# Kernel optimization log

Hardware: AMD Instinct MI355X
Metric: run time of the kernel (lower is better)

The kernel has to match this reference:

```python
import jax, jax.numpy as jnp
import numpy as np

DT_SCALE = 0.01  # time grid = arange(T) * 0.01, i.e. t in [0, 0.99]


def setup_inputs() -> dict:
    key = jax.random.key(0)
    k1, k2, k3 = jax.random.split(key, 3)
    latents, hidden = 128, 256
    S, N, T = 4, 1024, 100
    first_point = jax.random.normal(k1, (S, N, latents), dtype=jnp.float32)
    time_steps_to_predict = jnp.arange(T, dtype=jnp.float32) * DT_SCALE
    # ODEFunc MLP params (Glorot-ish scaling so tanh stays in a sane range)
    W1 = jax.random.normal(k2, (latents, hidden), dtype=jnp.float32) / np.sqrt(latents)
    b1 = jnp.zeros((hidden,), dtype=jnp.float32)
    W2 = jax.random.normal(k3, (hidden, latents), dtype=jnp.float32) / np.sqrt(hidden)
    b2 = jnp.zeros((latents,), dtype=jnp.float32)
    return {
        "first_point": first_point,
        "time_steps_to_predict": time_steps_to_predict,
        "W1": W1, "b1": b1, "W2": W2, "b2": b2,
    }


def reference(first_point, time_steps_to_predict, W1, b1, W2, b2):
    # ode_func: dy/dt = tanh(y @ W1 + b1) @ W2 + b2 (time-autonomous MLP)
    def f(y):
        return jnp.tanh(y @ W1 + b1) @ W2 + b2

    # torchdiffeq fixed-step 'rk4': one classical RK4 step per output interval.
    t0s = time_steps_to_predict[:-1]
    t1s = time_steps_to_predict[1:]

    def rk4_step(y, ts):
        t0, t1 = ts
        dt = t1 - t0
        half = dt * 0.5
        k1 = f(y)
        k2 = f(y + half * k1)
        k3 = f(y + half * k2)
        k4 = f(y + dt * k3)
        y1 = y + (dt / 6.0) * (k1 + 2.0 * k2 + 2.0 * k3 + k4)
        return y1, y1

    _, ys = jax.lax.scan(rk4_step, first_point, (t0s, t1s))  # [T-1, S, N, D]
    pred_y = jnp.concatenate([first_point[None], ys], axis=0)  # [T, S, N, D]
    # permute(1, 2, 0, 3): [T, S, N, D] -> [S, N, T, D]
    return jnp.transpose(pred_y, (1, 2, 0, 3))
```

## Files before the change

### kernel.cpp

```cpp
#include <hip/hip_runtime.h>
#include <hip/hip_bf16.h>

typedef __attribute__((ext_vector_type(8))) short v8s;
typedef __attribute__((ext_vector_type(4))) float f4;

#define MFMA16(a, b, c) __builtin_amdgcn_mfma_f32_16x16x32_bf16((a), (b), (c), 0, 0, 0)

__device__ __forceinline__ float bf2f(unsigned short u) {
    return __uint_as_float(((unsigned)u) << 16);
}
__device__ __forceinline__ unsigned short f2bf(float x) {
    unsigned u = __float_as_uint(x);
    unsigned r = 0x7FFFu + ((u >> 16) & 1u);
    return (unsigned short)((u + r) >> 16);
}
__device__ __forceinline__ unsigned pack_bf16_2(float a, float b) {
    float2 t; t.x = a; t.y = b;
    union { __hip_bfloat162 h; unsigned u; } cv;
    cv.h = __float22bfloat162_rn(t);
    return cv.u;
}
__device__ __forceinline__ float tanh_scaled(float zs) {
    float u = __builtin_amdgcn_exp2f(zs);
    float r = __builtin_amdgcn_rcpf(u + 1.0f);
    return __builtin_fmaf(-2.0f, r, 1.0f);
}
__device__ __forceinline__ float ldin(const void* p, int i, bool f32) {
    return f32 ? ((const float*)p)[i] : bf2f(((const unsigned short*)p)[i]);
}

#define BROWS 16
#define TSTEPS 100
#define DLAT 128
#define DHID 256
#define HSTR 264
#define HBUF (BROWS * HSTR)
#define TANH_C 2.885390081777927f

__global__ __launch_bounds__(256, 4)
void prep_w21(const void* __restrict__ ts, const void* __restrict__ W1,
              const void* __restrict__ W2, const void* __restrict__ b2,
              void* __restrict__ ws) {
    const bool m32 = fabsf(((const float*)ts)[1] - 0.01f) < 0.004f;
    const int i = blockIdx.x;
    const int j = threadIdx.x;
    float acc = 0.f;
    for (int m = 0; m < DLAT; ++m)
        acc = __builtin_fmaf(ldin(W2, i * DLAT + m, m32), ldin(W1, m * DHID + j, m32), acc);
    ((unsigned short*)ws)[i * DHID + j] = f2bf(TANH_C * acc);
    if (i == 0) {
        float a2 = 0.f;
        for (int m = 0; m < DLAT; ++m)
            a2 = __builtin_fmaf(ldin(b2, m, m32), ldin(W1, m * DHID + j, m32), a2);
        ((float*)((char*)ws + DHID * DHID * 2))[j] = TANH_C * a2;
    }
}

__global__ __launch_bounds__(512, 2)
void ode_rk4_kernel(const void* __restrict__ fp,
                    const void* __restrict__ ts,
                    const void* __restrict__ W1,
                    const void* __restrict__ b1,
                    const void* __restrict__ W2,
                    const void* __restrict__ b2,
                    const void* __restrict__ ws,
                    void* __restrict__ out) {
    __shared__ unsigned short hB[2 * HBUF];
    __shared__ float tsL[TSTEPS];

    const bool m32 = fabsf(((const float*)ts)[1] - 0.01f) < 0.004f;

    const int tid = threadIdx.x;
    const int w = tid >> 6;
    const int lane = tid & 63;
    const int pp = lane & 15;
    const int qq = lane >> 4;
    const int R0 = blockIdx.x * BROWS;

    if (tid < TSTEPS) tsL[tid] = ldin(ts, tid, m32);

    v8s w2f[8];
#pragma unroll
    for (int kt = 0; kt < 8; ++kt) {
        v8s f;
#pragma unroll
        for (int j = 0; j < 8; ++j)
            f[j] = (short)f2bf(ldin(W2, (kt * 32 + qq * 8 + j) * DLAT + 16 * w + pp, m32));
        w2f[kt] = f;
    }
    const unsigned short* w21p = (const unsigned short*)ws;
    v8s w21f[8][2];
#pragma unroll
    for (int kt = 0; kt < 8; ++kt)
#pragma unroll
        for (int nt = 0; nt < 2; ++nt) {
            v8s f;
#pragma unroll
            for (int j = 0; j < 8; ++j)
                f[j] = (short)w21p[(kt * 32 + qq * 8 + j) * DHID + 32 * w + nt * 16 + pp];
            w21f[kt][nt] = f;
        }
    const float* b2w1p = (const float*)((const char*)ws + DHID * DHID * 2);
    const float bz0 = b2w1p[32 * w + pp];
    const float bz1 = b2w1p[32 * w + 16 + pp];
    const float b2v = ldin(b2, 16 * w + pp, m32);

    const int sA = (pp >> 1) & 7;
    int hAoff[8];
#pragma unroll
    for (int kt = 0; kt < 8; ++kt)
        hAoff[kt] = pp * HSTR + (((4 * kt + qq) ^ sA) << 3);
    const int pb = pp >> 3, pw = pp & 7;
    const int s0 = (2 * qq) & 7, s1 = (2 * qq + 1) & 7;
    int hoff[2][2];
    hoff[0][0] = (((4 * w + pb) ^ s0) << 3) + pw;
    hoff[0][1] = (((4 * w + 2 + pb) ^ s0) << 3) + pw;
    hoff[1][0] = (((4 * w + pb) ^ s1) << 3) + pw;
    hoff[1][1] = (((4 * w + 2 + pb) ^ s1) << 3) + pw;

    {
        int row = tid >> 5, ch = tid & 31;
        int sw = (row >> 1) & 7;
        unsigned short* dst = hB + row * HSTR + (((ch >> 1) ^ sw) << 3) + (ch & 1) * 4;
        if (m32) {
            float4 v = *((const float4*)((const float*)fp + (size_t)(R0 + row) * DLAT) + ch);
            *((float4*)((float*)out + ((size_t)(R0 + row) * TSTEPS) * DLAT) + ch) = v;
            ushort4 b; b.x = f2bf(v.x); b.y = f2bf(v.y); b.z = f2bf(v.z); b.w = f2bf(v.w);
            *(ushort4*)dst = b;
        } else {
            const unsigned short* fpu = (const unsigned short*)fp;
            ushort4 v = *((const ushort4*)(fpu + (size_t)(R0 + row) * DLAT) + ch);
            *((ushort4*)((unsigned short*)out + ((size_t)(R0 + row) * TSTEPS) * DLAT) + ch) = v;
            *(ushort4*)dst = v;
        }
    }

    const int c2 = 16 * w + pp;
    float yreg[4];
    size_t ob[4];
#pragma unroll
    for (int r = 0; r < 4; ++r) {
        yreg[r] = ldin(fp, (R0 + 4 * qq + r) * DLAT + c2, m32);
        ob[r] = ((size_t)(R0 + 4 * qq + r) * TSTEPS) * DLAT + c2;
    }

    v8s w1f[4][2];
#pragma unroll
    for (int kt = 0; kt < 4; ++kt)
#pragma unroll
        for (int nt = 0; nt < 2; ++nt) {
            v8s f;
#pragma unroll
            for (int j = 0; j < 8; ++j)
                f[j] = (short)f2bf(TANH_C * ldin(W1, (kt * 32 + qq * 8 + j) * DHID + 32 * w + nt * 16 + pp, m32));
            w1f[kt][nt] = f;
        }
    const float b1s0 = TANH_C * ldin(b1, 32 * w + pp, m32);
    const float b1s1 = TANH_C * ldin(b1, 32 * w + 16 + pp, m32);

    __syncthreads();
    f4 a0 = {0.f, 0.f, 0.f, 0.f}, a1 = {0.f, 0.f, 0.f, 0.f};
#pragma unroll
    for (int kt = 0; kt < 4; ++kt) {
        v8s a = *(const v8s*)(hB + hAoff[kt]);
        a0 = MFMA16(a, w1f[kt][0], a0);
        a1 = MFMA16(a, w1f[kt][1], a1);
    }
    float zs[8];
#pragma unroll
    for (int r = 0; r < 4; ++r) {
        zs[r] = a0[r] + b1s0;
        zs[4 + r] = a1[r] + b1s1;
    }
#pragma unroll
    for (int r = 0; r < 4; ++r) {
        unsigned pu = pack_bf16_2(tanh_scaled(zs[r]), tanh_scaled(zs[4 + r]));
        unsigned short* hp = hB + HBUF + (4 * qq + r) * HSTR;
        hp[hoff[r >> 1][0]] = (unsigned short)pu;
        hp[hoff[r >> 1][1]] = (unsigned short)(pu >> 16);
    }

    for (int t = 0; t < TSTEPS - 1; ++t) {
        const float dt = tsL[t + 1] - tsL[t];
        const float half = 0.5f * dt;
        const float d6 = dt * (1.0f / 6.0f);
        float ksum[4] = {0.f, 0.f, 0.f, 0.f};
        float zsum[8] = {0.f, 0.f, 0.f, 0.f, 0.f, 0.f, 0.f, 0.f};
#pragma unroll
        for (int e = 0; e < 4; ++e) {
            const int rb = (e & 1) ^ 1;
            const int wb = e & 1;
            __syncthreads();
            const unsigned short* hbase = hB + rb * HBUF;
            f4 az0 = {0.f, 0.f, 0.f, 0.f}, az1 = {0.f, 0.f, 0.f, 0.f}, ak = {0.f, 0.f, 0.f, 0.f};
#pragma unroll
            for (int kt = 0; kt < 8; ++kt) {
                v8s a = *(const v8s*)(hbase + hAoff[kt]);
                az0 = MFMA16(a, w21f[kt][0], az0);
                az1 = MFMA16(a, w21f[kt][1], az1);
                ak  = MFMA16(a, w2f[kt], ak);
            }
            const float wgt = (e == 0 || e == 3) ? 1.0f : 2.0f;
            const float cc = (e == 2) ? dt : half;
            float zt[8];
#pragma unroll
            for (int r = 0; r < 4; ++r) {
                float kv = ak[r] + b2v;
                ksum[r] = __builtin_fmaf(wgt, kv, ksum[r]);
                float kz0 = az0[r] + bz0;
                float kz1 = az1[r] + bz1;
                zsum[r]     = __builtin_fmaf(wgt, kz0, zsum[r]);
                zsum[4 + r] = __builtin_fmaf(wgt, kz1, zsum[4 + r]);
                if (e < 3) {
                    zt[r]     = __builtin_fmaf(cc, kz0, zs[r]);
                    zt[4 + r] = __builtin_fmaf(cc, kz1, zs[4 + r]);
                }
            }
            if (e == 3) {
#pragma unroll
                for (int j = 0; j < 8; ++j) {
                    zs[j] = __builtin_fmaf(d6, zsum[j], zs[j]);
                    zt[j] = zs[j];
                }
#pragma unroll
                for (int r = 0; r < 4; ++r)
                    yreg[r] = __builtin_fmaf(d6, ksum[r], yreg[r]);
            }
            unsigned short* wbase = hB + wb * HBUF;
#pragma unroll
            for (int r = 0; r < 4; ++r) {
                unsigned pu = pack_bf16_2(tanh_scaled(zt[r]), tanh_scaled(zt[4 + r]));
                unsigned short* hp = wbase + (4 * qq + r) * HSTR;
                hp[hoff[r >> 1][0]] = (unsigned short)pu;
                hp[hoff[r >> 1][1]] = (unsigned short)(pu >> 16);
            }
        }
        if (m32) {
            float* op = (float*)out;
#pragma unroll
            for (int r = 0; r < 4; ++r)
                op[ob[r] + (size_t)(t + 1) * DLAT] = yreg[r];
        } else {
            unsigned short* op = (unsigned short*)out;
#pragma unroll
            for (int r = 0; r < 4; ++r)
                op[ob[r] + (size_t)(t + 1) * DLAT] = f2bf(yreg[r]);
        }
    }
}

extern "C" void kernel_launch(void* const* d_in, const int* in_sizes, int n_in,
                              void* d_out, int out_size, void* d_ws, size_t ws_size,
                              hipStream_t stream) {
    (void)in_sizes; (void)n_in; (void)out_size; (void)ws_size;
    prep_w21<<<DHID, DHID, 0, stream>>>(d_in[1], d_in[2], d_in[4], d_in[5], d_ws);
    ode_rk4_kernel<<<256, 512, 0, stream>>>(d_in[0], d_in[1], d_in[2], d_in[3],
                                            d_in[4], d_in[5], d_ws, d_out);
}
```

Before: 547.6 us.

## Halve block to four waves, each computing double-width output tiles

The RK4 kernel now launches 256 threads (4 waves) per 16-row block instead of 512. Each wave covers 64 hidden columns and 32 latent columns, so it keeps twice as many weight fragments in registers and reuses each A-fragment LDS load across more MFMAs. Tanh and writeback are interleaved per N-tile, the LDS row padding is removed in favour of a new XOR swizzle, and the bf16 input path uses wider vector loads. This cuts barrier participants and LDS reads per MFMA but greatly raises register pressure. With launch bounds of 1 block per SM, occupancy across the 256 blocks may drop.

```diff
diff --git a/kernel.cpp b/kernel.cpp
--- a/kernel.cpp
+++ b/kernel.cpp
@@ -2,6 +2,7 @@
 #include <hip/hip_bf16.h>
 
 typedef __attribute__((ext_vector_type(8))) short v8s;
+typedef __attribute__((ext_vector_type(8))) unsigned short u8s;
 typedef __attribute__((ext_vector_type(4))) float f4;
 
 #define MFMA16(a, b, c) __builtin_amdgcn_mfma_f32_16x16x32_bf16((a), (b), (c), 0, 0, 0)
@@ -33,7 +34,7 @@
 #define TSTEPS 100
 #define DLAT 128
 #define DHID 256
-#define HSTR 264
+#define HSTR 256
 #define HBUF (BROWS * HSTR)
 #define TANH_C 2.885390081777927f
 
@@ -56,7 +57,7 @@
     }
 }
 
-__global__ __launch_bounds__(512, 2)
+__global__ __launch_bounds__(256, 1)
 void ode_rk4_kernel(const void* __restrict__ fp,
                     const void* __restrict__ ts,
                     const void* __restrict__ W1,
@@ -79,172 +80,195 @@
 
     if (tid < TSTEPS) tsL[tid] = ldin(ts, tid, m32);
 
-    v8s w2f[8];
-#pragma unroll
-    for (int kt = 0; kt < 8; ++kt) {
-        v8s f;
-#pragma unroll
-        for (int j = 0; j < 8; ++j)
-            f[j] = (short)f2bf(ldin(W2, (kt * 32 + qq * 8 + j) * DLAT + 16 * w + pp, m32));
-        w2f[kt] = f;
-    }
     const unsigned short* w21p = (const unsigned short*)ws;
-    v8s w21f[8][2];
+    v8s w21f[8][4];
 #pragma unroll
     for (int kt = 0; kt < 8; ++kt)
 #pragma unroll
-        for (int nt = 0; nt < 2; ++nt) {
+        for (int nt = 0; nt < 4; ++nt) {
             v8s f;
 #pragma unroll
             for (int j = 0; j < 8; ++j)
-                f[j] = (short)w21p[(kt * 32 + qq * 8 + j) * DHID + 32 * w + nt * 16 + pp];
+                f[j] = (short)w21p[(kt * 32 + qq * 8 + j) * DHID + 64 * w + nt * 16 + pp];
             w21f[kt][nt] = f;
         }
+    v8s w2f[8][2];
+#pragma unroll
+    for (int kt = 0; kt < 8; ++kt)
+#pragma unroll
+        for (int u = 0; u < 2; ++u) {
+            v8s f;
+#pragma unroll
+            for (int j = 0; j < 8; ++j)
+                f[j] = (short)f2bf(ldin(W2, (kt * 32 + qq * 8 + j) * DLAT + 32 * w + u * 16 + pp, m32));
+            w2f[kt][u] = f;
+        }
     const float* b2w1p = (const float*)((const char*)ws + DHID * DHID * 2);
-    const float bz0 = b2w1p[32 * w + pp];
-    const float bz1 = b2w1p[32 * w + 16 + pp];
-    const float b2v = ldin(b2, 16 * w + pp, m32);
-
-    const int sA = (pp >> 1) & 7;
+    float bz[4];
+#pragma unroll
+    for (int nt = 0; nt < 4; ++nt) bz[nt] = b2w1p[64 * w + 16 * nt + pp];
+    float b2v[2];
+#pragma unroll
+    for (int u = 0; u < 2; ++u) b2v[u] = ldin(b2, 32 * w + 16 * u + pp, m32);
+
+    const int spp = (pp & 7) ^ ((pp & 8) >> 2);
     int hAoff[8];
 #pragma unroll
     for (int kt = 0; kt < 8; ++kt)
-        hAoff[kt] = pp * HSTR + (((4 * kt + qq) ^ sA) << 3);
+        hAoff[kt] = pp * HSTR + (((4 * kt + qq) ^ spp) << 3);
     const int pb = pp >> 3, pw = pp & 7;
-    const int s0 = (2 * qq) & 7, s1 = (2 * qq + 1) & 7;
-    int hoff[2][2];
-    hoff[0][0] = (((4 * w + pb) ^ s0) << 3) + pw;
-    hoff[0][1] = (((4 * w + 2 + pb) ^ s0) << 3) + pw;
-    hoff[1][0] = (((4 * w + pb) ^ s1) << 3) + pw;
-    hoff[1][1] = (((4 * w + 2 + pb) ^ s1) << 3) + pw;
-
-    {
-        int row = tid >> 5, ch = tid & 31;
-        int sw = (row >> 1) & 7;
-        unsigned short* dst = hB + row * HSTR + (((ch >> 1) ^ sw) << 3) + (ch & 1) * 4;
-        if (m32) {
+    int hoffs[4][4];
+#pragma unroll
+    for (int nt = 0; nt < 4; ++nt)
+#pragma unroll
+        for (int r = 0; r < 4; ++r) {
+            int row = 4 * qq + r;
+            int s = (row & 7) ^ ((row & 8) >> 2);
+            hoffs[nt][r] = row * HSTR + (((8 * w + 2 * nt + pb) ^ s) << 3) + pw;
+        }
+
+    if (m32) {
+#pragma unroll
+        for (int rr = 0; rr < 2; ++rr) {
+            int row = (tid >> 5) + 8 * rr, ch = tid & 31;
+            int s = (row & 7) ^ ((row & 8) >> 2);
             float4 v = *((const float4*)((const float*)fp + (size_t)(R0 + row) * DLAT) + ch);
             *((float4*)((float*)out + ((size_t)(R0 + row) * TSTEPS) * DLAT) + ch) = v;
             ushort4 b; b.x = f2bf(v.x); b.y = f2bf(v.y); b.z = f2bf(v.z); b.w = f2bf(v.w);
-            *(ushort4*)dst = b;
-        } else {
-            const unsigned short* fpu = (const unsigned short*)fp;
-            ushort4 v = *((const ushort4*)(fpu + (size_t)(R0 + row) * DLAT) + ch);
-            *((ushort4*)((unsigned short*)out + ((size_t)(R0 + row) * TSTEPS) * DLAT) + ch) = v;
-            *(ushort4*)dst = v;
-        }
-    }
-
-    const int c2 = 16 * w + pp;
-    float yreg[4];
-    size_t ob[4];
-#pragma unroll
-    for (int r = 0; r < 4; ++r) {
-        yreg[r] = ldin(fp, (R0 + 4 * qq + r) * DLAT + c2, m32);
-        ob[r] = ((size_t)(R0 + 4 * qq + r) * TSTEPS) * DLAT + c2;
-    }
-
-    v8s w1f[4][2];
+            *(ushort4*)(hB + row * HSTR + (((ch >> 1) ^ s) << 3) + (ch & 1) * 4) = b;
+        }
+    } else {
+        int row = tid >> 4, ch = tid & 15;
+        int s = (row & 7) ^ ((row & 8) >> 2);
+        const unsigned short* fpu = (const unsigned short*)fp;
+        u8s v = *((const u8s*)(fpu + (size_t)(R0 + row) * DLAT) + ch);
+        *((u8s*)((unsigned short*)out + ((size_t)(R0 + row) * TSTEPS) * DLAT) + ch) = v;
+        *(u8s*)(hB + row * HSTR + ((ch ^ s) << 3)) = v;
+    }
+
+    const int cy0 = 32 * w + pp;
+    float yreg[8];
+    int ob[8];
+#pragma unroll
+    for (int r = 0; r < 4; ++r)
+#pragma unroll
+        for (int u = 0; u < 2; ++u) {
+            yreg[4 * u + r] = ldin(fp, (R0 + 4 * qq + r) * DLAT + cy0 + 16 * u, m32);
+            ob[4 * u + r] = (R0 + 4 * qq + r) * (TSTEPS * DLAT) + cy0 + 16 * u;
+        }
+
+    v8s w1f[4][4];
 #pragma unroll
     for (int kt = 0; kt < 4; ++kt)
 #pragma unroll
-        for (int nt = 0; nt < 2; ++nt) {
+        for (int nt = 0; nt < 4; ++nt) {
             v8s f;
 #pragma unroll
             for (int j = 0; j < 8; ++j)
-                f[j] = (short)f2bf(TANH_C * ldin(W1, (kt * 32 + qq * 8 + j) * DHID + 32 * w + nt * 16 + pp, m32));
+                f[j] = (short)f2bf(TANH_C * ldin(W1, (kt * 32 + qq * 8 + j) * DHID + 64 * w + nt * 16 + pp, m32));
             w1f[kt][nt] = f;
         }
-    const float b1s0 = TANH_C * ldin(b1, 32 * w + pp, m32);
-    const float b1s1 = TANH_C * ldin(b1, 32 * w + 16 + pp, m32);
+    float b1s[4];
+#pragma unroll
+    for (int nt = 0; nt < 4; ++nt) b1s[nt] = TANH_C * ldin(b1, 64 * w + 16 * nt + pp, m32);
 
     __syncthreads();
-    f4 a0 = {0.f, 0.f, 0.f, 0.f}, a1 = {0.f, 0.f, 0.f, 0.f};
-#pragma unroll
-    for (int kt = 0; kt < 4; ++kt) {
-        v8s a = *(const v8s*)(hB + hAoff[kt]);
-        a0 = MFMA16(a, w1f[kt][0], a0);
-        a1 = MFMA16(a, w1f[kt][1], a1);
-    }
-    float zs[8];
-#pragma unroll
-    for (int r = 0; r < 4; ++r) {
-        zs[r] = a0[r] + b1s0;
-        zs[4 + r] = a1[r] + b1s1;
-    }
-#pragma unroll
-    for (int r = 0; r < 4; ++r) {
-        unsigned pu = pack_bf16_2(tanh_scaled(zs[r]), tanh_scaled(zs[4 + r]));
-        unsigned short* hp = hB + HBUF + (4 * qq + r) * HSTR;
-        hp[hoff[r >> 1][0]] = (unsigned short)pu;
-        hp[hoff[r >> 1][1]] = (unsigned short)(pu >> 16);
+    float zs[16];
+    {
+        v8s a0[4];
+#pragma unroll
+        for (int kt = 0; kt < 4; ++kt) a0[kt] = *(const v8s*)(hB + hAoff[kt]);
+#pragma unroll
+        for (int nt = 0; nt < 4; ++nt) {
+            f4 az = {0.f, 0.f, 0.f, 0.f};
+#pragma unroll
+            for (int kt = 0; kt < 4; ++kt) az = MFMA16(a0[kt], w1f[kt][nt], az);
+            float th[4];
+#pragma unroll
+            for (int r = 0; r < 4; ++r) {
+                zs[nt * 4 + r] = az[r] + b1s[nt];
+                th[r] = tanh_scaled(zs[nt * 4 + r]);
+            }
+            unsigned short* wp = hB + HBUF;
+            unsigned p0 = pack_bf16_2(th[0], th[1]);
+            unsigned p1 = pack_bf16_2(th[2], th[3]);
+            wp[hoffs[nt][0]] = (unsigned short)p0;
+            wp[hoffs[nt][1]] = (unsigned short)(p0 >> 16);
+            wp[hoffs[nt][2]] = (unsigned short)p1;
+            wp[hoffs[nt][3]] = (unsigned short)(p1 >> 16);
+        }
     }
 
     for (int t = 0; t < TSTEPS - 1; ++t) {
         const float dt = tsL[t + 1] - tsL[t];
         const float half = 0.5f * dt;
         const float d6 = dt * (1.0f / 6.0f);
-        float ksum[4] = {0.f, 0.f, 0.f, 0.f};
-        float zsum[8] = {0.f, 0.f, 0.f, 0.f, 0.f, 0.f, 0.f, 0.f};
+        float ksum[8] = {0.f, 0.f, 0.f, 0.f, 0.f, 0.f, 0.f, 0.f};
+        float zsum[16];
+#pragma unroll
+        for (int j = 0; j < 16; ++j) zsum[j] = 0.f;
 #pragma unroll
         for (int e = 0; e < 4; ++e) {
             const int rb = (e & 1) ^ 1;
             const int wb = e & 1;
             __syncthreads();
             const unsigned short* hbase = hB + rb * HBUF;
-            f4 az0 = {0.f, 0.f, 0.f, 0.f}, az1 = {0.f, 0.f, 0.f, 0.f}, ak = {0.f, 0.f, 0.f, 0.f};
-#pragma unroll
-            for (int kt = 0; kt < 8; ++kt) {
-                v8s a = *(const v8s*)(hbase + hAoff[kt]);
-                az0 = MFMA16(a, w21f[kt][0], az0);
-                az1 = MFMA16(a, w21f[kt][1], az1);
-                ak  = MFMA16(a, w2f[kt], ak);
-            }
+            unsigned short* wbase = hB + wb * HBUF;
+            v8s a[8];
+#pragma unroll
+            for (int kt = 0; kt < 8; ++kt) a[kt] = *(const v8s*)(hbase + hAoff[kt]);
             const float wgt = (e == 0 || e == 3) ? 1.0f : 2.0f;
             const float cc = (e == 2) ? dt : half;
-            float zt[8];
+#pragma unroll
+            for (int nt = 0; nt < 4; ++nt) {
+                f4 az = {0.f, 0.f, 0.f, 0.f};
+#pragma unroll
+                for (int kt = 0; kt < 8; ++kt) az = MFMA16(a[kt], w21f[kt][nt], az);
+                float th[4];
+#pragma unroll
+                for (int r = 0; r < 4; ++r) {
+                    float kz = az[r] + bz[nt];
+                    zsum[nt * 4 + r] = __builtin_fmaf(wgt, kz, zsum[nt * 4 + r]);
+                    float ztv;
+                    if (e < 3) {
+                        ztv = __builtin_fmaf(cc, kz, zs[nt * 4 + r]);
+                    } else {
+                        zs[nt * 4 + r] = __builtin_fmaf(d6, zsum[nt * 4 + r], zs[nt * 4 + r]);
+                        ztv = zs[nt * 4 + r];
+                    }
+                    th[r] = tanh_scaled(ztv);
+                }
+                unsigned p0 = pack_bf16_2(th[0], th[1]);
+                unsigned p1 = pack_bf16_2(th[2], th[3]);
+                wbase[hoffs[nt][0]] = (unsigned short)p0;
+                wbase[hoffs[nt][1]] = (unsigned short)(p0 >> 16);
+                wbase[hoffs[nt][2]] = (unsigned short)p1;
+                wbase[hoffs[nt][3]] = (unsigned short)(p1 >> 16);
+            }
+            f4 ak0 = {0.f, 0.f, 0.f, 0.f}, ak1 = {0.f, 0.f, 0.f, 0.f};
+#pragma unroll
+            for (int kt = 0; kt < 8; ++kt) {
+                ak0 = MFMA16(a[kt], w2f[kt][0], ak0);
+                ak1 = MFMA16(a[kt], w2f[kt][1], ak1);
+            }
 #pragma unroll
             for (int r = 0; r < 4; ++r) {
-                float kv = ak[r] + b2v;
-                ksum[r] = __builtin_fmaf(wgt, kv, ksum[r]);
-                float kz0 = az0[r] + bz0;
-                float kz1 = az1[r] + bz1;
-                zsum[r]     = __builtin_fmaf(wgt, kz0, zsum[r]);
-                zsum[4 + r] = __builtin_fmaf(wgt, kz1, zsum[4 + r]);
-                if (e < 3) {
-                    zt[r]     = __builtin_fmaf(cc, kz0, zs[r]);
-                    zt[4 + r] = __builtin_fmaf(cc, kz1, zs[4 + r]);
-                }
-            }
-            if (e == 3) {
-#pragma unroll
-                for (int j = 0; j < 8; ++j) {
-                    zs[j] = __builtin_fmaf(d6, zsum[j], zs[j]);
-                    zt[j] = zs[j];
-                }
-#pragma unroll
-                for (int r = 0; r < 4; ++r)
-                    yreg[r] = __builtin_fmaf(d6, ksum[r], yreg[r]);
-            }
-            unsigned short* wbase = hB + wb * HBUF;
-#pragma unroll
-            for (int r = 0; r < 4; ++r) {
-                unsigned pu = pack_bf16_2(tanh_scaled(zt[r]), tanh_scaled(zt[4 + r]));
-                unsigned short* hp = wbase + (4 * qq + r) * HSTR;
-                hp[hoff[r >> 1][0]] = (unsigned short)pu;
-                hp[hoff[r >> 1][1]] = (unsigned short)(pu >> 16);
-            }
-        }
+                ksum[r]     = __builtin_fmaf(wgt, ak0[r] + b2v[0], ksum[r]);
+                ksum[4 + r] = __builtin_fmaf(wgt, ak1[r] + b2v[1], ksum[4 + r]);
+            }
+        }
+#pragma unroll
+        for (int j = 0; j < 8; ++j) yreg[j] = __builtin_fmaf(d6, ksum[j], yreg[j]);
         if (m32) {
             float* op = (float*)out;
 #pragma unroll
-            for (int r = 0; r < 4; ++r)
-                op[ob[r] + (size_t)(t + 1) * DLAT] = yreg[r];
+            for (int j = 0; j < 8; ++j)
+                op[ob[j] + (t + 1) * DLAT] = yreg[j];
         } else {
             unsigned short* op = (unsigned short*)out;
 #pragma unroll
-            for (int r = 0; r < 4; ++r)
-                op[ob[r] + (size_t)(t + 1) * DLAT] = f2bf(yreg[r]);
+            for (int j = 0; j < 8; ++j)
+                op[ob[j] + (t + 1) * DLAT] = f2bf(yreg[j]);
         }
     }
 }
@@ -254,6 +278,6 @@
                               hipStream_t stream) {
     (void)in_sizes; (void)n_in; (void)out_size; (void)ws_size;
     prep_w21<<<DHID, DHID, 0, stream>>>(d_in[1], d_in[2], d_in[4], d_in[5], d_ws);
-    ode_rk4_kernel<<<256, 512, 0, stream>>>(d_in[0], d_in[1], d_in[2], d_in[3],
+    ode_rk4_kernel<<<256, 256, 0, stream>>>(d_in[0], d_in[1], d_in[2], d_in[3],
                                             d_in[4], d_in[5], d_ws, d_out);
 }
```

After: 683.2 us. 24.7% more time.
